# Optimization experiments

Measured on AMD Instinct MI355X. Metric: run time of the kernel, lower is better.

## Reference

```python
import jax, jax.numpy as jnp
import numpy as np

NUM_HEADS = 12
MASK_BIAS = -1000.0


def setup_inputs() -> dict:
    key = jax.random.key(0)
    k1, k2, k3, k4 = jax.random.split(key, 4)
    B, N, C = 2, 2048, 768
    x = jax.random.normal(k1, (B, N, C), dtype=jnp.float32)
    # key-padding mask: 1.0 = masked-out position (gets -1000 bias), 0.0 = visible
    mask = jax.random.randint(k2, (B, N), 0, 2).astype(jnp.float32)
    qkv_w = jax.random.normal(k3, (3 * C, C), dtype=jnp.float32) * (1.0 / np.sqrt(C))
    proj_w = jax.random.normal(k4, (C, C), dtype=jnp.float32) * (1.0 / np.sqrt(C))
    proj_b = jnp.zeros((C,), dtype=jnp.float32)
    return {"x": x, "mask": mask, "qkv_w": qkv_w, "proj_w": proj_w, "proj_b": proj_b}


def reference(x, mask, qkv_w, proj_w, proj_b):
    B, N, C = x.shape
    H = NUM_HEADS
    D = C // H
    scale = D ** (-0.5)
    # qkv: Linear without bias -> [B, N, 3C] -> [3, B, H, N, D]
    qkv = (x @ qkv_w.T).reshape(B, N, 3, H, D).transpose(2, 0, 3, 1, 4)
    q, k, v = qkv[0], qkv[1], qkv[2]
    # scores [B, H, N, N]
    attn = jnp.einsum("bhqd,bhkd->bhqk", q, k) * scale
    attn = attn + mask[:, None, None, :] * MASK_BIAS
    attn = jax.nn.softmax(attn, axis=-1)
    out = jnp.einsum("bhqk,bhkd->bhqd", attn, v)  # [B, H, N, D]
    out = out.transpose(0, 2, 1, 3).reshape(B, N, C)
    return out @ proj_w.T + proj_b
```

## Files before the change

### kernel.cpp

```cpp
#include <hip/hip_runtime.h>

typedef __bf16 bf16_t;
typedef __bf16 bf16x8 __attribute__((ext_vector_type(8)));
typedef float f32x4 __attribute__((ext_vector_type(4)));

#define NUM_B 2
#define NUM_H 12
#define SEQ_N 2048
#define DIM_C 768
#define HEAD_D 64
#define BH_CNT (NUM_B * NUM_H)
#define MTOK (NUM_B * SEQ_N)
#define QSCALE 0.1803368801111137f

#define AS1(p) ((const __attribute__((address_space(1))) void*)(p))
#define AS3(p) ((__attribute__((address_space(3))) void*)(p))


__global__ __launch_bounds__(256) void cvt_scan_kernel(
    const float* __restrict__ s0, const float* __restrict__ s1,
    const float* __restrict__ s2, const float* __restrict__ msk,
    bf16_t* __restrict__ d0, bf16_t* __restrict__ d1, bf16_t* __restrict__ d2,
    int* __restrict__ src, bf16_t* __restrict__ wp, int* __restrict__ cnts,
    int nb0, int nb1, int nb2) {
  __shared__ int psum[256];
  const int blk = blockIdx.x;
  const int t = threadIdx.x;
  if (blk >= nb0 + nb1 + nb2) {
    const int b = blk - (nb0 + nb1 + nb2);
    const float* mb = msk + (size_t)b * SEQ_N;
    int vis[8], c = 0;
#pragma unroll
    for (int j = 0; j < 8; ++j) {
      vis[j] = (mb[t * 8 + j] == 0.0f) ? 1 : 0;
      c += vis[j];
    }
    psum[t] = c;
    __syncthreads();
    for (int off = 1; off < 256; off <<= 1) {
      int v = (t >= off) ? psum[t - off] : 0;
      __syncthreads();
      psum[t] += v;
      __syncthreads();
    }
    const int total = psum[255];
    int vpos = psum[t] - c;
    int mpos = total + (t * 8 - (psum[t] - c));
#pragma unroll
    for (int j = 0; j < 8; ++j) {
      const int tok = t * 8 + j;
      if (vis[j]) {
        src[b * SEQ_N + vpos] = b * SEQ_N + tok;
        wp[b * SEQ_N + vpos] = (bf16_t)1.0f;
        ++vpos;
      } else {
        src[b * SEQ_N + mpos] = b * SEQ_N + tok;
        wp[b * SEQ_N + mpos] = (bf16_t)0.0f;
        ++mpos;
      }
    }
    if (t == 0) {
      cnts[b * 2] = (total + 63) & ~63;
      cnts[b * 2 + 1] = total;
    }
    return;
  }
  const float* sp;
  bf16_t* dp;
  size_t off;
  if (blk < nb0) {
    sp = s0; dp = d0; off = (size_t)blk * 2048;
  } else if (blk < nb0 + nb1) {
    sp = s1; dp = d1; off = (size_t)(blk - nb0) * 2048;
  } else {
    sp = s2; dp = d2; off = (size_t)(blk - nb0 - nb1) * 2048;
  }
  const size_t i = off + (size_t)t * 8;
  float4 f0 = *reinterpret_cast<const float4*>(&sp[i]);
  float4 f1 = *reinterpret_cast<const float4*>(&sp[i + 4]);
  union { ushort4 u; bf16_t h[4]; } p0, p1;
  p0.h[0] = (bf16_t)f0.x; p0.h[1] = (bf16_t)f0.y;
  p0.h[2] = (bf16_t)f0.z; p0.h[3] = (bf16_t)f0.w;
  p1.h[0] = (bf16_t)f1.x; p1.h[1] = (bf16_t)f1.y;
  p1.h[2] = (bf16_t)f1.z; p1.h[3] = (bf16_t)f1.w;
  *reinterpret_cast<ushort4*>(&dp[i]) = p0.u;
  *reinterpret_cast<ushort4*>(&dp[i + 4]) = p1.u;
}

__global__ __launch_bounds__(256, 3) void gemm_qkv_kernel(
    const bf16_t* __restrict__ A, const bf16_t* __restrict__ W,
    const int* __restrict__ src, const int* __restrict__ cnts,
    bf16_t* __restrict__ out) {
  __shared__ __align__(16) bf16_t As[2][128 * 32];
  __shared__ __align__(16) bf16_t Bs[2][128 * 32];

  const int tid = threadIdx.x;
  const int wave = tid >> 6, lane = tid & 63;
  const int quad = lane >> 4, l16 = lane & 15;
  const int m0 = blockIdx.y * 128, n0 = blockIdx.x * 128;
  const int wm = (wave >> 1) * 64, wn = (wave & 1) * 64;
  const bool isQ = (n0 < DIM_C);

  if (!isQ) {
    const int b = m0 >> 11;
    if ((m0 & 2047) >= cnts[b * 2]) return;
  }

  f32x4 acc[4][4] = {};

  const int srow = tid >> 2;
  const int scol = ((tid & 3) ^ ((tid >> 3) & 3)) * 8;
  int ar0, ar1;
  if (isQ) {
    ar0 = m0 + srow;
    ar1 = m0 + srow + 64;
  } else {
    ar0 = src[m0 + srow];
    ar1 = src[m0 + srow + 64];
  }
  const bf16_t* gA0 = A + (size_t)ar0 * DIM_C + scol;
  const bf16_t* gA1 = A + (size_t)ar1 * DIM_C + scol;
  const bf16_t* gB0 = W + (size_t)(n0 + srow) * DIM_C + scol;
  const bf16_t* gB1 = W + (size_t)(n0 + srow + 64) * DIM_C + scol;
  const int lb = wave * 512;

  auto issue = [&](int buf, int k0) {
    __builtin_amdgcn_global_load_lds(AS1(gA0 + k0), AS3(&As[buf][lb]), 16, 0, 0);
    __builtin_amdgcn_global_load_lds(AS1(gA1 + k0), AS3(&As[buf][lb + 2048]), 16, 0, 0);
    __builtin_amdgcn_global_load_lds(AS1(gB0 + k0), AS3(&Bs[buf][lb]), 16, 0, 0);
    __builtin_amdgcn_global_load_lds(AS1(gB1 + k0), AS3(&Bs[buf][lb + 2048]), 16, 0, 0);
  };

  issue(0, 0);
  int cur = 0;
  const int sw = (l16 >> 1) & 3;
  for (int step = 0; step < DIM_C / 32; ++step) {
    __syncthreads();
    if (step + 1 < DIM_C / 32) issue(cur ^ 1, (step + 1) * 32);

    bf16x8 aF[4], bF[4];
#pragma unroll
    for (int mi = 0; mi < 4; ++mi)
      aF[mi] = *reinterpret_cast<const bf16x8*>(
          &As[cur][(wm + mi * 16 + l16) * 32 + ((quad ^ sw) * 8)]);
#pragma unroll
    for (int ni = 0; ni < 4; ++ni)
      bF[ni] = *reinterpret_cast<const bf16x8*>(
          &Bs[cur][(wn + ni * 16 + l16) * 32 + ((quad ^ sw) * 8)]);
#pragma unroll
    for (int mi = 0; mi < 4; ++mi)
#pragma unroll
      for (int ni = 0; ni < 4; ++ni)
        acc[mi][ni] = __builtin_amdgcn_mfma_f32_16x16x32_bf16(aF[mi], bF[ni],
                                                              acc[mi][ni], 0, 0, 0);
    cur ^= 1;
  }

  const size_t per = (size_t)BH_CNT * SEQ_N * HEAD_D;
#pragma unroll
  for (int mi = 0; mi < 4; ++mi) {
#pragma unroll
    for (int ni = 0; ni < 4; ++ni) {
      const int gmB = m0 + wm + mi * 16 + quad * 4;
      const int gn = n0 + wn + ni * 16 + l16;
      const int b = gmB >> 11;
      if (isQ) {
        const int h = gn >> 6, d = gn & 63;
#pragma unroll
        for (int r = 0; r < 4; ++r) {
          const int gm = gmB + r;
          const int tok = gm & 2047;
          out[(((size_t)((gm >> 11) * NUM_H + h) * SEQ_N + tok) * HEAD_D + d)] =
              (bf16_t)(acc[mi][ni][r] * QSCALE);
        }
      } else if (n0 < 2 * DIM_C) {
        const int rem = gn - DIM_C;
        const int hh = rem >> 6, d = rem & 63;
        const int posm = gmB & 2047;
        const int bh = b * NUM_H + hh;
        const size_t base = per +
            (((size_t)(bh * 128 + (posm >> 4)) * 2 + (d >> 5)) * 512 +
             ((d >> 3) & 3) * 128 + (d & 7));
        const int l16k = posm & 15;
#pragma unroll
        for (int r = 0; r < 4; ++r)
          out[base + (size_t)(l16k + r) * 8] = (bf16_t)acc[mi][ni][r];
      } else {
        const int rem = gn - 2 * DIM_C;
        const int hh = rem >> 6, d = rem & 63;
        const int posm = gmB & 2047;
        const int bh = b * NUM_H + hh;
        const int count = cnts[b * 2 + 1];
        const size_t base = 2 * per +
            (((size_t)(bh * 64 + (posm >> 5)) * 4 + (d >> 4)) * 512 +
             ((posm >> 3) & 3) * 128 + (d & 15) * 8 + (posm & 7));
        union { ushort4 u; bf16_t h4[4]; } pk;
#pragma unroll
        for (int r = 0; r < 4; ++r)
          pk.h4[r] = (posm + r < count) ? (bf16_t)acc[mi][ni][r] : (bf16_t)0.0f;
        *reinterpret_cast<ushort4*>(&out[base]) = pk.u;
      }
    }
  }
}

__global__ __launch_bounds__(256, 3) void gemm_proj_kernel(
    const bf16_t* __restrict__ A, const bf16_t* __restrict__ W,
    const float* __restrict__ bias, float* __restrict__ out) {
  __shared__ __align__(16) bf16_t As[2][128 * 32];
  __shared__ __align__(16) bf16_t Bs[2][128 * 32];

  const int tid = threadIdx.x;
  const int wave = tid >> 6, lane = tid & 63;
  const int quad = lane >> 4, l16 = lane & 15;
  const int m0 = blockIdx.y * 128, n0 = blockIdx.x * 128;
  const int wm = (wave >> 1) * 64, wn = (wave & 1) * 64;

  f32x4 acc[4][4] = {};

  const int srow = tid >> 2;
  const int scol = ((tid & 3) ^ ((tid >> 3) & 3)) * 8;
  const bf16_t* gA0 = A + (size_t)(m0 + srow) * DIM_C + scol;
  const bf16_t* gA1 = A + (size_t)(m0 + srow + 64) * DIM_C + scol;
  const bf16_t* gB0 = W + (size_t)(n0 + srow) * DIM_C + scol;
  const bf16_t* gB1 = W + (size_t)(n0 + srow + 64) * DIM_C + scol;
  const int lb = wave * 512;

  auto issue = [&](int buf, int k0) {
    __builtin_amdgcn_global_load_lds(AS1(gA0 + k0), AS3(&As[buf][lb]), 16, 0, 0);
    __builtin_amdgcn_global_load_lds(AS1(gA1 + k0), AS3(&As[buf][lb + 2048]), 16, 0, 0);
    __builtin_amdgcn_global_load_lds(AS1(gB0 + k0), AS3(&Bs[buf][lb]), 16, 0, 0);
    __builtin_amdgcn_global_load_lds(AS1(gB1 + k0), AS3(&Bs[buf][lb + 2048]), 16, 0, 0);
  };

  issue(0, 0);
  int cur = 0;
  const int sw = (l16 >> 1) & 3;
  for (int step = 0; step < DIM_C / 32; ++step) {
    __syncthreads();
    if (step + 1 < DIM_C / 32) issue(cur ^ 1, (step + 1) * 32);

    bf16x8 aF[4], bF[4];
#pragma unroll
    for (int mi = 0; mi < 4; ++mi)
      aF[mi] = *reinterpret_cast<const bf16x8*>(
          &As[cur][(wm + mi * 16 + l16) * 32 + ((quad ^ sw) * 8)]);
#pragma unroll
    for (int ni = 0; ni < 4; ++ni)
      bF[ni] = *reinterpret_cast<const bf16x8*>(
          &Bs[cur][(wn + ni * 16 + l16) * 32 + ((quad ^ sw) * 8)]);
#pragma unroll
    for (int mi = 0; mi < 4; ++mi)
#pragma unroll
      for (int ni = 0; ni < 4; ++ni)
        acc[mi][ni] = __builtin_amdgcn_mfma_f32_16x16x32_bf16(aF[mi], bF[ni],
                                                              acc[mi][ni], 0, 0, 0);
    cur ^= 1;
  }

#pragma unroll
  for (int mi = 0; mi < 4; ++mi) {
#pragma unroll
    for (int ni = 0; ni < 4; ++ni) {
      const int gmB = m0 + wm + mi * 16 + quad * 4;
      const int gn = n0 + wn + ni * 16 + l16;
      const float bv = bias[gn];
#pragma unroll
      for (int r = 0; r < 4; ++r)
        out[(size_t)(gmB + r) * DIM_C + gn] = acc[mi][ni][r] + bv;
    }
  }
}

__global__ __launch_bounds__(512, 4) void attn_kernel(
    const bf16_t* __restrict__ q, const bf16_t* __restrict__ kfr,
    const bf16_t* __restrict__ vfr, const bf16_t* __restrict__ wp,
    const int* __restrict__ cnts, bf16_t* __restrict__ ctx) {
  __shared__ __align__(16) bf16_t Ps[8][1024];
  __shared__ float Om[4][16][65];
  __shared__ float Lm[64];

  const int tid = threadIdx.x;
  const int wave = tid >> 6, lane = tid & 63;
  const int quad = lane >> 4, l16 = lane & 15;
  const int g = wave >> 2, wsub = wave & 3;
  const int bh = blockIdx.y;
  const int b = bh / NUM_H, h = bh - b * NUM_H;
  const int q0 = blockIdx.x * 64 + wsub * 16;
  const int cntPad = cnts[b * 2];
  const int half = ((cntPad >> 1) + 63) & ~63;
  const int kbeg = g ? half : 0;
  const int kend = g ? cntPad : half;

  const bf16_t* qb = q + (size_t)bh * SEQ_N * HEAD_D;
  const bf16_t* kbase = kfr + (size_t)bh * 128 * 1024;
  const bf16_t* vbase = vfr + (size_t)bh * 64 * 2048;
  const bf16_t* wb = wp + (size_t)b * SEQ_N;

  bf16x8 qf[2];
#pragma unroll
  for (int ks = 0; ks < 2; ++ks)
    qf[ks] = *reinterpret_cast<const bf16x8*>(
        &qb[(size_t)(q0 + l16) * HEAD_D + ks * 32 + quad * 8]);

  f32x4 acc[4] = {};
  f32x4 acc_l = {};

  const int swz = l16 & 7;
  const int psbase = wave * 1024 + l16 * 64;

  for (int key0 = kbeg; key0 < kend; key0 += 64) {
    const bf16_t* kc_p = kbase + (size_t)(key0 >> 4) * 1024 + lane * 8;
    bf16x8 kf[4][2];
#pragma unroll
    for (int kt = 0; kt < 4; ++kt) {
      kf[kt][0] = *reinterpret_cast<const bf16x8*>(kc_p + kt * 1024);
      kf[kt][1] = *reinterpret_cast<const bf16x8*>(kc_p + kt * 1024 + 512);
    }
    const bf16_t* vc_p = vbase + (size_t)(key0 >> 5) * 2048 + lane * 8;
    bf16x8 vf[2][4];
#pragma unroll
    for (int kc = 0; kc < 2; ++kc)
#pragma unroll
      for (int dt = 0; dt < 4; ++dt)
        vf[kc][dt] = *reinterpret_cast<const bf16x8*>(vc_p + kc * 2048 + dt * 512);

    f32x4 s[4];
#pragma unroll
    for (int kt = 0; kt < 4; ++kt) {
      f32x4 z = {0.0f, 0.0f, 0.0f, 0.0f};
      z = __builtin_amdgcn_mfma_f32_16x16x32_bf16(kf[kt][0], qf[0], z, 0, 0, 0);
      s[kt] = __builtin_amdgcn_mfma_f32_16x16x32_bf16(kf[kt][1], qf[1], z, 0, 0, 0);
    }

#pragma unroll
    for (int kt = 0; kt < 4; ++kt) {
      union { ushort4 u; bf16_t h4[4]; } pk;
      pk.h4[0] = (bf16_t)exp2f(s[kt][0]);
      pk.h4[1] = (bf16_t)exp2f(s[kt][1]);
      pk.h4[2] = (bf16_t)exp2f(s[kt][2]);
      pk.h4[3] = (bf16_t)exp2f(s[kt][3]);
      const int c = kt * 2 + (quad >> 1);
      *reinterpret_cast<ushort4*>(
          &Ps[0][psbase + ((c ^ swz) << 3) + ((quad & 1) << 2)]) = pk.u;
    }

    bf16x8 pf0 = *reinterpret_cast<const bf16x8*>(
        &Ps[0][psbase + ((quad ^ swz) << 3)]);
    bf16x8 pf1 = *reinterpret_cast<const bf16x8*>(
        &Ps[0][psbase + (((4 + quad) ^ swz) << 3)]);
    bf16x8 wf0 = *reinterpret_cast<const bf16x8*>(&wb[key0 + quad * 8]);
    bf16x8 wf1 = *reinterpret_cast<const bf16x8*>(&wb[key0 + 32 + quad * 8]);
    acc_l = __builtin_amdgcn_mfma_f32_16x16x32_bf16(pf0, wf0, acc_l, 0, 0, 0);
    acc_l = __builtin_amdgcn_mfma_f32_16x16x32_bf16(pf1, wf1, acc_l, 0, 0, 0);

#pragma unroll
    for (int dt = 0; dt < 4; ++dt) {
      acc[dt] = __builtin_amdgcn_mfma_f32_16x16x32_bf16(pf0, vf[0][dt], acc[dt], 0, 0, 0);
      acc[dt] = __builtin_amdgcn_mfma_f32_16x16x32_bf16(pf1, vf[1][dt], acc[dt], 0, 0, 0);
    }
  }

  if (g == 0) {
#pragma unroll
    for (int dt = 0; dt < 4; ++dt)
#pragma unroll
      for (int r = 0; r < 4; ++r)
        Om[wsub][quad * 4 + r][dt * 16 + l16] = acc[dt][r];
    if (l16 == 0) {
#pragma unroll
      for (int r = 0; r < 4; ++r) Lm[wsub * 16 + quad * 4 + r] = acc_l[r];
    }
  }
  __syncthreads();
  if (g == 1) {
    float rl[4];
#pragma unroll
    for (int r = 0; r < 4; ++r)
      rl[r] = 1.0f / (acc_l[r] + Lm[wsub * 16 + quad * 4 + r]);
#pragma unroll
    for (int dt = 0; dt < 4; ++dt)
#pragma unroll
      for (int r = 0; r < 4; ++r) {
        const int tok = q0 + quad * 4 + r;
        const float val =
            (acc[dt][r] + Om[wsub][quad * 4 + r][dt * 16 + l16]) * rl[r];
        ctx[((size_t)b * SEQ_N + tok) * DIM_C + h * HEAD_D + dt * 16 + l16] =
            (bf16_t)val;
      }
  }
}

extern "C" void kernel_launch(void* const* d_in, const int* in_sizes, int n_in,
                              void* d_out, int out_size, void* d_ws,
                              size_t ws_size, hipStream_t stream) {
  const float* x = (const float*)d_in[0];
  const float* mask = (const float*)d_in[1];
  const float* qkv_w = (const float*)d_in[2];
  const float* proj_w = (const float*)d_in[3];
  const float* proj_b = (const float*)d_in[4];
  float* out = (float*)d_out;

  const size_t nx = (size_t)MTOK * DIM_C;
  const size_t nqw = (size_t)3 * DIM_C * DIM_C;
  const size_t npw = (size_t)DIM_C * DIM_C;
  const size_t per = (size_t)BH_CNT * SEQ_N * HEAD_D;

  bf16_t* xb = (bf16_t*)d_ws;
  bf16_t* qwb = xb + nx;
  bf16_t* pwb = qwb + nqw;
  bf16_t* wpb = pwb + npw;
  int* srcb = (int*)(wpb + MTOK);
  int* cntsb = srcb + MTOK;
  bf16_t* qkv = (bf16_t*)(cntsb + 8);
  bf16_t* ctx = qkv + 3 * per;

  const int nb0 = (int)(nx / 2048), nb1 = (int)(nqw / 2048),
            nb2 = (int)(npw / 2048);

  cvt_scan_kernel<<<nb0 + nb1 + nb2 + NUM_B, 256, 0, stream>>>(
      x, qkv_w, proj_w, mask, xb, qwb, pwb, srcb, wpb, cntsb, nb0, nb1, nb2);
  gemm_qkv_kernel<<<dim3(3 * DIM_C / 128, MTOK / 128), 256, 0, stream>>>(
      xb, qwb, srcb, cntsb, qkv);
  attn_kernel<<<dim3(SEQ_N / 64, BH_CNT), 512, 0, stream>>>(
      qkv, qkv + per, qkv + 2 * per, wpb, cntsb, ctx);
  gemm_proj_kernel<<<dim3(DIM_C / 128, MTOK / 128), 256, 0, stream>>>(
      ctx, pwb, proj_b, out);
}
```

Before: 157.7 us.

## Stage K/V tiles into LDS with double-buffered async global_load_lds in attention

Each of the four waves in a group previously loaded its own copy of the K and V fragments from global memory. Now the waves cooperatively copy each 64-key K/V tile into LDS using async global_load_lds, double-buffered so the next tile loads while the current one is computed. This removes the redundant global reads and overlaps memory with MFMA work. In exchange it adds a block-wide barrier every iteration and raises LDS use to 80 KB per block, which cannot fit the 4 blocks per CU implied by the launch bounds and so lowers occupancy.

```diff
diff --git a/kernel.cpp b/kernel.cpp
--- a/kernel.cpp
+++ b/kernel.cpp
@@ -276,9 +276,12 @@
     const bf16_t* __restrict__ q, const bf16_t* __restrict__ kfr,
     const bf16_t* __restrict__ vfr, const bf16_t* __restrict__ wp,
     const int* __restrict__ cnts, bf16_t* __restrict__ ctx) {
-  __shared__ __align__(16) bf16_t Ps[8][1024];
-  __shared__ float Om[4][16][65];
-  __shared__ float Lm[64];
+  __shared__ __align__(16) char smem[81920];
+  bf16_t* Ks = (bf16_t*)smem;
+  bf16_t* Vs = (bf16_t*)(smem + 32768);
+  bf16_t* Ps = (bf16_t*)(smem + 65536);
+  float* Om = (float*)smem;
+  float* Lm = (float*)(smem + 16640);
 
   const int tid = threadIdx.x;
   const int wave = tid >> 6, lane = tid & 63;
@@ -291,6 +294,7 @@
   const int half = ((cntPad >> 1) + 63) & ~63;
   const int kbeg = g ? half : 0;
   const int kend = g ? cntPad : half;
+  const int nIter = half >> 6;
 
   const bf16_t* qb = q + (size_t)bh * SEQ_N * HEAD_D;
   const bf16_t* kbase = kfr + (size_t)bh * 128 * 1024;
@@ -306,67 +310,83 @@
   f32x4 acc[4] = {};
   f32x4 acc_l = {};
 
+  auto stage = [&](int buf, int key0) {
+    const bf16_t* kp = kbase + (size_t)(key0 >> 4) * 1024 + wsub * 1024 + lane * 8;
+    const bf16_t* vp = vbase + (size_t)(key0 >> 5) * 2048 + wsub * 1024 + lane * 8;
+    bf16_t* kd = Ks + (g * 2 + buf) * 4096 + wsub * 1024;
+    bf16_t* vd = Vs + (g * 2 + buf) * 4096 + wsub * 1024;
+    __builtin_amdgcn_global_load_lds(AS1(kp), AS3(kd), 16, 0, 0);
+    __builtin_amdgcn_global_load_lds(AS1(kp + 512), AS3(kd + 512), 16, 0, 0);
+    __builtin_amdgcn_global_load_lds(AS1(vp), AS3(vd), 16, 0, 0);
+    __builtin_amdgcn_global_load_lds(AS1(vp + 512), AS3(vd + 512), 16, 0, 0);
+  };
+
   const int swz = l16 & 7;
   const int psbase = wave * 1024 + l16 * 64;
 
-  for (int key0 = kbeg; key0 < kend; key0 += 64) {
-    const bf16_t* kc_p = kbase + (size_t)(key0 >> 4) * 1024 + lane * 8;
-    bf16x8 kf[4][2];
-#pragma unroll
-    for (int kt = 0; kt < 4; ++kt) {
-      kf[kt][0] = *reinterpret_cast<const bf16x8*>(kc_p + kt * 1024);
-      kf[kt][1] = *reinterpret_cast<const bf16x8*>(kc_p + kt * 1024 + 512);
-    }
-    const bf16_t* vc_p = vbase + (size_t)(key0 >> 5) * 2048 + lane * 8;
-    bf16x8 vf[2][4];
-#pragma unroll
-    for (int kc = 0; kc < 2; ++kc)
-#pragma unroll
-      for (int dt = 0; dt < 4; ++dt)
-        vf[kc][dt] = *reinterpret_cast<const bf16x8*>(vc_p + kc * 2048 + dt * 512);
-
-    f32x4 s[4];
-#pragma unroll
-    for (int kt = 0; kt < 4; ++kt) {
-      f32x4 z = {0.0f, 0.0f, 0.0f, 0.0f};
-      z = __builtin_amdgcn_mfma_f32_16x16x32_bf16(kf[kt][0], qf[0], z, 0, 0, 0);
-      s[kt] = __builtin_amdgcn_mfma_f32_16x16x32_bf16(kf[kt][1], qf[1], z, 0, 0, 0);
-    }
-
-#pragma unroll
-    for (int kt = 0; kt < 4; ++kt) {
-      union { ushort4 u; bf16_t h4[4]; } pk;
-      pk.h4[0] = (bf16_t)exp2f(s[kt][0]);
-      pk.h4[1] = (bf16_t)exp2f(s[kt][1]);
-      pk.h4[2] = (bf16_t)exp2f(s[kt][2]);
-      pk.h4[3] = (bf16_t)exp2f(s[kt][3]);
-      const int c = kt * 2 + (quad >> 1);
-      *reinterpret_cast<ushort4*>(
-          &Ps[0][psbase + ((c ^ swz) << 3) + ((quad & 1) << 2)]) = pk.u;
-    }
-
-    bf16x8 pf0 = *reinterpret_cast<const bf16x8*>(
-        &Ps[0][psbase + ((quad ^ swz) << 3)]);
-    bf16x8 pf1 = *reinterpret_cast<const bf16x8*>(
-        &Ps[0][psbase + (((4 + quad) ^ swz) << 3)]);
-    bf16x8 wf0 = *reinterpret_cast<const bf16x8*>(&wb[key0 + quad * 8]);
-    bf16x8 wf1 = *reinterpret_cast<const bf16x8*>(&wb[key0 + 32 + quad * 8]);
-    acc_l = __builtin_amdgcn_mfma_f32_16x16x32_bf16(pf0, wf0, acc_l, 0, 0, 0);
-    acc_l = __builtin_amdgcn_mfma_f32_16x16x32_bf16(pf1, wf1, acc_l, 0, 0, 0);
-
-#pragma unroll
-    for (int dt = 0; dt < 4; ++dt) {
-      acc[dt] = __builtin_amdgcn_mfma_f32_16x16x32_bf16(pf0, vf[0][dt], acc[dt], 0, 0, 0);
-      acc[dt] = __builtin_amdgcn_mfma_f32_16x16x32_bf16(pf1, vf[1][dt], acc[dt], 0, 0, 0);
-    }
-  }
-
+  if (kbeg < kend) stage(0, kbeg);
+  int buf = 0;
+  for (int i = 0; i < nIter; ++i) {
+    __syncthreads();
+    const int key0 = kbeg + i * 64;
+    const int nxt = key0 + 64;
+    if (nxt < kend) stage(buf ^ 1, nxt);
+
+    if (key0 < kend) {
+      const int base = (g * 2 + buf) * 4096;
+      f32x4 s[4];
+#pragma unroll
+      for (int kt = 0; kt < 4; ++kt) {
+        bf16x8 kf0 = *reinterpret_cast<const bf16x8*>(
+            &Ks[base + kt * 1024 + lane * 8]);
+        bf16x8 kf1 = *reinterpret_cast<const bf16x8*>(
+            &Ks[base + kt * 1024 + 512 + lane * 8]);
+        f32x4 z = {0.0f, 0.0f, 0.0f, 0.0f};
+        z = __builtin_amdgcn_mfma_f32_16x16x32_bf16(kf0, qf[0], z, 0, 0, 0);
+        s[kt] = __builtin_amdgcn_mfma_f32_16x16x32_bf16(kf1, qf[1], z, 0, 0, 0);
+      }
+
+#pragma unroll
+      for (int kt = 0; kt < 4; ++kt) {
+        union { ushort4 u; bf16_t h4[4]; } pk;
+        pk.h4[0] = (bf16_t)exp2f(s[kt][0]);
+        pk.h4[1] = (bf16_t)exp2f(s[kt][1]);
+        pk.h4[2] = (bf16_t)exp2f(s[kt][2]);
+        pk.h4[3] = (bf16_t)exp2f(s[kt][3]);
+        const int c = kt * 2 + (quad >> 1);
+        *reinterpret_cast<ushort4*>(
+            &Ps[psbase + ((c ^ swz) << 3) + ((quad & 1) << 2)]) = pk.u;
+      }
+
+      bf16x8 pf0 = *reinterpret_cast<const bf16x8*>(
+          &Ps[psbase + ((quad ^ swz) << 3)]);
+      bf16x8 pf1 = *reinterpret_cast<const bf16x8*>(
+          &Ps[psbase + (((4 + quad) ^ swz) << 3)]);
+      bf16x8 wf0 = *reinterpret_cast<const bf16x8*>(&wb[key0 + quad * 8]);
+      bf16x8 wf1 = *reinterpret_cast<const bf16x8*>(&wb[key0 + 32 + quad * 8]);
+      acc_l = __builtin_amdgcn_mfma_f32_16x16x32_bf16(pf0, wf0, acc_l, 0, 0, 0);
+      acc_l = __builtin_amdgcn_mfma_f32_16x16x32_bf16(pf1, wf1, acc_l, 0, 0, 0);
+
+#pragma unroll
+      for (int dt = 0; dt < 4; ++dt) {
+        bf16x8 vf0 = *reinterpret_cast<const bf16x8*>(
+            &Vs[base + dt * 512 + lane * 8]);
+        bf16x8 vf1 = *reinterpret_cast<const bf16x8*>(
+            &Vs[base + 2048 + dt * 512 + lane * 8]);
+        acc[dt] = __builtin_amdgcn_mfma_f32_16x16x32_bf16(pf0, vf0, acc[dt], 0, 0, 0);
+        acc[dt] = __builtin_amdgcn_mfma_f32_16x16x32_bf16(pf1, vf1, acc[dt], 0, 0, 0);
+      }
+    }
+    buf ^= 1;
+  }
+
+  __syncthreads();
   if (g == 0) {
 #pragma unroll
     for (int dt = 0; dt < 4; ++dt)
 #pragma unroll
       for (int r = 0; r < 4; ++r)
-        Om[wsub][quad * 4 + r][dt * 16 + l16] = acc[dt][r];
+        Om[(wsub * 16 + quad * 4 + r) * 65 + dt * 16 + l16] = acc[dt][r];
     if (l16 == 0) {
 #pragma unroll
       for (int r = 0; r < 4; ++r) Lm[wsub * 16 + quad * 4 + r] = acc_l[r];
@@ -384,7 +404,8 @@
       for (int r = 0; r < 4; ++r) {
         const int tok = q0 + quad * 4 + r;
         const float val =
-            (acc[dt][r] + Om[wsub][quad * 4 + r][dt * 16 + l16]) * rl[r];
+            (acc[dt][r] + Om[(wsub * 16 + quad * 4 + r) * 65 + dt * 16 + l16]) *
+            rl[r];
         ctx[((size_t)b * SEQ_N + tok) * DIM_C + h * HEAD_D + dt * 16 + l16] =
             (bf16_t)val;
       }
```

Result: faster. 148.3 us (-6.0%).
